# Performance work log

Hardware: AMD Instinct MI355X
Metric: run time of the kernel (lower is better)

Reference implementation:

```python
import jax, jax.numpy as jnp
import numpy as np

N_NODES = 100000
N_EDGES = 1000000
IN_F = 64
HEADS = 4
OUT_C = 32  # per-head channels
EDGE_DIM = 16
NEG_SLOPE = 0.2


def setup_inputs() -> dict:
    key = jax.random.key(0)
    ks = jax.random.split(key, 10)
    x = jax.random.normal(ks[0], (N_NODES, IN_F), dtype=jnp.float32)
    edge_index = jax.random.randint(ks[1], (2, N_EDGES), 0, N_NODES, dtype=jnp.int64)
    edge_attr = jax.random.normal(ks[2], (N_EDGES, EDGE_DIM), dtype=jnp.float32)
    s = 1.0 / np.sqrt(IN_F)
    W = jax.random.normal(ks[3], (IN_F, HEADS * OUT_C), dtype=jnp.float32) * s
    W_edge = jax.random.normal(ks[4], (EDGE_DIM, HEADS * OUT_C), dtype=jnp.float32) * (1.0 / np.sqrt(EDGE_DIM))
    att_src = jax.random.normal(ks[5], (HEADS, OUT_C), dtype=jnp.float32) * (1.0 / np.sqrt(OUT_C))
    att_dst = jax.random.normal(ks[6], (HEADS, OUT_C), dtype=jnp.float32) * (1.0 / np.sqrt(OUT_C))
    att_edge = jax.random.normal(ks[7], (HEADS, OUT_C), dtype=jnp.float32) * (1.0 / np.sqrt(OUT_C))
    bias = jnp.zeros((HEADS * OUT_C,), dtype=jnp.float32)
    return {"x": x, "edge_index": edge_index, "edge_attr": edge_attr,
            "W": W, "W_edge": W_edge, "att_src": att_src, "att_dst": att_dst,
            "att_edge": att_edge, "bias": bias}


def reference(x, edge_index, edge_attr, W, W_edge, att_src, att_dst, att_edge, bias):
    # PyG GATConv with edge_dim, add_self_loops=False, concat=True.
    N = x.shape[0]
    src = edge_index[0]  # message source j
    dst = edge_index[1]  # message target i

    x_proj = (x @ W).reshape(N, HEADS, OUT_C)          # [N,H,C]
    a_src = jnp.einsum('nhc,hc->nh', x_proj, att_src)  # [N,H]
    a_dst = jnp.einsum('nhc,hc->nh', x_proj, att_dst)  # [N,H]

    e_proj = (edge_attr @ W_edge).reshape(-1, HEADS, OUT_C)  # [E,H,C]
    a_edge = jnp.einsum('ehc,hc->eh', e_proj, att_edge)      # [E,H]

    alpha = a_src[src] + a_dst[dst] + a_edge                 # [E,H]
    alpha = jax.nn.leaky_relu(alpha, NEG_SLOPE)

    # edge softmax grouped by destination node
    seg_max = jax.ops.segment_max(alpha, dst, num_segments=N)  # [N,H]
    alpha = jnp.exp(alpha - seg_max[dst])
    denom = jax.ops.segment_sum(alpha, dst, num_segments=N)    # [N,H]
    alpha = alpha / (denom[dst] + 1e-16)

    msg = x_proj[src] * alpha[:, :, None]                      # [E,H,C]
    out = jax.ops.segment_sum(msg, dst, num_segments=N)        # [N,H,C]
    return out.reshape(N, HEADS * OUT_C) + bias
```

## Files before the change

### kernel.cpp

```cpp
#include <hip/hip_runtime.h>
#include <hip/hip_fp16.h>


#define HC 128
#define NEG 0.2f
#define CH 16
#define K_SHIFT 6.0f
#define NBK 512
#define BSH 8
#define BMSK 255
#define BCAP 3584
#define EPB 4096

typedef __fp16 half2_t __attribute__((ext_vector_type(2)));

__device__ __forceinline__ unsigned short f2bf(float f) {
    unsigned u = __float_as_uint(f);
    return (unsigned short)((u + 0x7fffu + ((u >> 16) & 1u)) >> 16);
}
__device__ __forceinline__ unsigned pk_h2(float lo, float hi) {
    half2_t p = __builtin_amdgcn_cvt_pkrtz(lo, hi);
    union { half2_t h; unsigned u; } cv;
    cv.h = p;
    return cv.u;
}
__device__ __forceinline__ float h2f_bits(unsigned short bits) {
    __half_raw hr; hr.x = bits;
    return __half2float(*reinterpret_cast<__half*>(&hr));
}
__device__ __forceinline__ long ld_idx(const int* __restrict__ ei, long i, int m64) {
    return m64 ? (long)(((const long long*)ei)[i]) : (long)ei[i];
}
__device__ __forceinline__ int detect_m64(const int* __restrict__ ei, int* s_m64) {
    int t = threadIdx.x;
    if (t < 64) {
        unsigned long long bal = __ballot(ei[2 * t + 1] != 0);
        if (t == 0) *s_m64 = (bal == 0ull) ? 1 : 0;
    }
    __syncthreads();
    return *s_m64;
}

__global__ __launch_bounds__(1024) void k_bucket(
    const float* __restrict__ We, const float* __restrict__ ae,
    const float* __restrict__ eattr, const int* __restrict__ ei,
    int* __restrict__ bcur, unsigned* __restrict__ sdstg,
    uint2* __restrict__ aevstg, int E) {
    __shared__ float q_s[64];
    __shared__ int s_m64;
    __shared__ int hist[NBK];
    __shared__ int gb[NBK];
    int t = threadIdx.x;
    int m64 = detect_m64(ei, &s_m64);
    if (t < 64) {
        int dd = t >> 2, h = t & 3;
        float s = 0.f;
        for (int c = 0; c < 32; ++c)
            s += We[dd * HC + h * 32 + c] * ae[h * 32 + c];
        q_s[t] = s;
    }
    if (t < NBK) hist[t] = 0;
    __syncthreads();

    int base = blockIdx.x * EPB + t;
#pragma unroll
    for (int k = 0; k < 4; ++k) {
        int e = base + k * 1024;
        if (e < E) {
            int d = (int)ld_idx(ei, (long)E + e, m64);
            atomicAdd(&hist[d >> BSH], 1);
        }
    }
    __syncthreads();
    if (t < NBK) {
        int c = hist[t];
        gb[t] = c ? atomicAdd(&bcur[t], c) : 0;
        hist[t] = 0;
    }
    __syncthreads();

#pragma unroll
    for (int k = 0; k < 4; ++k) {
        int e = base + k * 1024;
        if (e >= E) continue;
        int d = (int)ld_idx(ei, (long)E + e, m64);
        int b = d >> BSH;
        int lr = atomicAdd(&hist[b], 1);
        int off = gb[b] + lr;
        if (off >= BCAP) continue;
        long s = ld_idx(ei, e, m64);
        const float4* pe = reinterpret_cast<const float4*>(eattr + (long)e * 16);
        float4 e0 = pe[0], e1 = pe[1], e2 = pe[2], e3 = pe[3];
        float ev[16] = {e0.x, e0.y, e0.z, e0.w, e1.x, e1.y, e1.z, e1.w,
                        e2.x, e2.y, e2.z, e2.w, e3.x, e3.y, e3.z, e3.w};
        float ov[4];
#pragma unroll
        for (int h = 0; h < 4; ++h) {
            float aev = 0.f;
#pragma unroll
            for (int dd = 0; dd < 16; ++dd) aev += ev[dd] * q_s[dd * 4 + h];
            ov[h] = aev;
        }
        int slot = b * BCAP + off;
        sdstg[slot] = (unsigned)s | ((unsigned)(d & BMSK) << 20);
        aevstg[slot] = make_uint2(pk_h2(ov[0], ov[1]), pk_h2(ov[2], ov[3]));
    }
}

__global__ void k_bscan(const int* __restrict__ bcur, int* __restrict__ bbase,
                        int* __restrict__ row, int N, int E) {
    int t = threadIdx.x;
    if (t >= 64) return;
    int v[8]; int sum = 0;
#pragma unroll
    for (int k = 0; k < 8; ++k) { v[k] = bcur[t * 8 + k]; sum += v[k]; }
    int s = sum;
#pragma unroll
    for (int off = 1; off < 64; off <<= 1) {
        int u = __shfl_up(s, off, 64);
        if (t >= off) s += u;
    }
    int run = s - sum;
#pragma unroll
    for (int k = 0; k < 8; ++k) { bbase[t * 8 + k] = run; run += v[k]; }
    if (t == 0) row[N] = E;
}

__global__ __launch_bounds__(512) void k_csr(
    const unsigned* __restrict__ sdstg, const uint2* __restrict__ aevstg,
    const int* __restrict__ bcur, const int* __restrict__ bbase,
    const float* __restrict__ a_src, const float* __restrict__ a_dst,
    int* __restrict__ row, uint4* __restrict__ srt, int N) {
    int b = blockIdx.x, t = threadIdx.x;
    __shared__ int deg_l[256];
    __shared__ int s_sc[256];
    __shared__ int pfx[256];
    if (t < 256) deg_l[t] = 0;
    __syncthreads();
    int cnt = bcur[b]; if (cnt > BCAP) cnt = BCAP;
    int base = bbase[b];

    int r[7];
    unsigned recs[7];
#pragma unroll
    for (int k = 0; k < 7; ++k) {
        int i = k * 512 + t;
        r[k] = -1; recs[k] = 0u;
        if (i < cnt) {
            unsigned sd = sdstg[b * BCAP + i];
            recs[k] = sd;
            r[k] = atomicAdd(&deg_l[(sd >> 20) & BMSK], 1);
        }
    }
    __syncthreads();
    int own = (t < 256) ? deg_l[t] : 0;
    if (t < 256) s_sc[t] = own;
    __syncthreads();
    for (int off = 1; off < 256; off <<= 1) {
        int xv = (t >= off && t < 256) ? s_sc[t - off] : 0;
        __syncthreads();
        if (t < 256) s_sc[t] += xv;
        __syncthreads();
    }
    if (t < 256) {
        int ex = s_sc[t] - own;
        pfx[t] = ex;
        int n = b * 256 + t;
        if (n <= N) row[n] = base + ex;
    }
    __syncthreads();

#pragma unroll
    for (int k = 0; k < 7; ++k) {
        int i = k * 512 + t;
        if (i >= cnt) continue;
        unsigned sd = recs[k];
        int dl = (sd >> 20) & BMSK;
        int s = (int)(sd & 0xFFFFFu);
        uint2 av = aevstg[b * BCAP + i];
        float4 s4 = *reinterpret_cast<const float4*>(a_src + (long)s * 4);
        float4 d4 = *reinterpret_cast<const float4*>(a_dst + (long)(b * 256 + dl) * 4);
        float lf[4];
        lf[0] = s4.x + d4.x + h2f_bits((unsigned short)(av.x & 0xffffu));
        lf[1] = s4.y + d4.y + h2f_bits((unsigned short)(av.x >> 16));
        lf[2] = s4.z + d4.z + h2f_bits((unsigned short)(av.y & 0xffffu));
        lf[3] = s4.w + d4.w + h2f_bits((unsigned short)(av.y >> 16));
        float exv[4];
#pragma unroll
        for (int h = 0; h < 4; ++h) {
            float v = (lf[h] > 0.f) ? lf[h] : NEG * lf[h];
            exv[h] = __expf(v - K_SHIFT);
        }
        int pos = base + pfx[dl] + r[k];
        srt[pos] = make_uint4((unsigned)s, pk_h2(exv[0], exv[1]),
                              pk_h2(exv[2], exv[3]), 0u);
    }
}

__global__ __launch_bounds__(256) void k_proj(
    const float* __restrict__ x, const float* __restrict__ W,
    const float* __restrict__ as_, const float* __restrict__ ad_,
    unsigned short* __restrict__ xp, float* __restrict__ a_src,
    float* __restrict__ a_dst, int N) {
    __shared__ float x_s[64][68];
    int t = threadIdx.x;
    int n0 = blockIdx.x * 64;
#pragma unroll
    for (int i = 0; i < 4; ++i) {
        int fl = i * 256 + t;
        int node = fl >> 4, f4 = fl & 15;
        float4 v = make_float4(0.f, 0.f, 0.f, 0.f);
        if (n0 + node < N)
            v = *reinterpret_cast<const float4*>(&x[(long)(n0 + node) * 64 + f4 * 4]);
        x_s[f4 * 4 + 0][node] = v.x;
        x_s[f4 * 4 + 1][node] = v.y;
        x_s[f4 * 4 + 2][node] = v.z;
        x_s[f4 * 4 + 3][node] = v.w;
    }
    __syncthreads();

    int c = t & 31;
    int nd = t >> 5;
    const float4* __restrict__ W4 = reinterpret_cast<const float4*>(W);
    float acc[8][4];
#pragma unroll
    for (int i = 0; i < 8; ++i)
#pragma unroll
        for (int j = 0; j < 4; ++j) acc[i][j] = 0.f;

#pragma unroll 8
    for (int k = 0; k < 64; ++k) {
        float4 w4 = W4[k * 32 + c];
        float4 xa = *reinterpret_cast<const float4*>(&x_s[k][nd * 8]);
        float4 xb = *reinterpret_cast<const float4*>(&x_s[k][nd * 8 + 4]);
        float xv[8] = {xa.x, xa.y, xa.z, xa.w, xb.x, xb.y, xb.z, xb.w};
#pragma unroll
        for (int i = 0; i < 8; ++i) {
            acc[i][0] += xv[i] * w4.x;
            acc[i][1] += xv[i] * w4.y;
            acc[i][2] += xv[i] * w4.z;
            acc[i][3] += xv[i] * w4.w;
        }
    }

    float4 s4 = *reinterpret_cast<const float4*>(&as_[c * 4]);
    float4 d4 = *reinterpret_cast<const float4*>(&ad_[c * 4]);
#pragma unroll
    for (int i = 0; i < 8; ++i) {
        int node = n0 + nd * 8 + i;
        if (node < N) {
            ushort4 o;
            o.x = f2bf(acc[i][0]); o.y = f2bf(acc[i][1]);
            o.z = f2bf(acc[i][2]); o.w = f2bf(acc[i][3]);
            *reinterpret_cast<ushort4*>(&xp[(long)node * HC + c * 4]) = o;
        }
        float ps = acc[i][0] * s4.x + acc[i][1] * s4.y + acc[i][2] * s4.z + acc[i][3] * s4.w;
        float pd = acc[i][0] * d4.x + acc[i][1] * d4.y + acc[i][2] * d4.z + acc[i][3] * d4.w;
#pragma unroll
        for (int off = 1; off < 8; off <<= 1) {
            ps += __shfl_xor(ps, off, 64);
            pd += __shfl_xor(pd, off, 64);
        }
        if ((c & 7) == 0 && node < N) {
            int h = c >> 3;
            a_src[(long)node * 4 + h] = ps;
            a_dst[(long)node * 4 + h] = pd;
        }
    }
}

__global__ __launch_bounds__(128) void k_gather(
    const int* __restrict__ row, const uint4* __restrict__ srt,
    const char* __restrict__ xpc, const float* __restrict__ bias,
    float* __restrict__ out, int N) {
    int wid = threadIdx.x >> 6;
    int lane = threadIdx.x & 63;
    int n = blockIdx.x * 2 + wid;
    if (n >= N) return;
    int beg = row[n], end = row[n + 1];
    int h_s = lane & 3, e_s = lane >> 2;
    int par = lane >> 5;
    int cl = lane & 31;
    int h_a = cl >> 3;
    float l = 0.f;
    float acc[4] = {0.f, 0.f, 0.f, 0.f};

    __shared__ float s_ex[2][CH][4];
    __shared__ int s_off[2][CH];
    __shared__ float s_l[2][4];

    for (int cs = beg; cs < end; cs += CH) {
        int cnt = end - cs;
        if (cnt > CH) cnt = CH;
        float ex = 0.f;
        if (e_s < cnt) {
            uint4 r = srt[cs + e_s];
            if (h_s == 0) s_off[wid][e_s] = (int)(r.x << 8);
            unsigned pr = (h_s & 2) ? r.z : r.y;
            unsigned bits = (h_s & 1) ? (pr >> 16) : (pr & 0xffffu);
            ex = h2f_bits((unsigned short)bits);
        }
        s_ex[wid][e_s][h_s] = ex;
        float se = ex;
        se += __shfl_xor(se, 4, 64);
        se += __shfl_xor(se, 8, 64);
        se += __shfl_xor(se, 16, 64);
        se += __shfl_xor(se, 32, 64);
        l += se;
        int j = 0;
        for (; j + 4 <= cnt; j += 4) {
            int ea0 = j + par, ea1 = j + 2 + par;
            int o0 = s_off[wid][ea0], o1 = s_off[wid][ea1];
            float w0 = s_ex[wid][ea0][h_a], w1 = s_ex[wid][ea1][h_a];
            uint2 v0 = *reinterpret_cast<const uint2*>(xpc + o0 + cl * 8);
            uint2 v1 = *reinterpret_cast<const uint2*>(xpc + o1 + cl * 8);
            acc[0] += w0 * __uint_as_float(v0.x << 16);
            acc[1] += w0 * __uint_as_float(v0.x & 0xffff0000u);
            acc[2] += w0 * __uint_as_float(v0.y << 16);
            acc[3] += w0 * __uint_as_float(v0.y & 0xffff0000u);
            acc[0] += w1 * __uint_as_float(v1.x << 16);
            acc[1] += w1 * __uint_as_float(v1.x & 0xffff0000u);
            acc[2] += w1 * __uint_as_float(v1.y << 16);
            acc[3] += w1 * __uint_as_float(v1.y & 0xffff0000u);
        }
        for (; j < cnt; j += 2) {
            int e = j + par;
            bool act = e < cnt;
            int o = s_off[wid][act ? e : j];
            float w = act ? s_ex[wid][e][h_a] : 0.f;
            uint2 v = *reinterpret_cast<const uint2*>(xpc + o + cl * 8);
            acc[0] += w * __uint_as_float(v.x << 16);
            acc[1] += w * __uint_as_float(v.x & 0xffff0000u);
            acc[2] += w * __uint_as_float(v.y << 16);
            acc[3] += w * __uint_as_float(v.y & 0xffff0000u);
        }
    }
    if (lane < 4) s_l[wid][h_s] = l;
#pragma unroll
    for (int k = 0; k < 4; ++k) acc[k] += __shfl_xor(acc[k], 32, 64);
    if (par == 0) {
        float d = s_l[wid][h_a] + 1e-16f;
        float4 b4 = *reinterpret_cast<const float4*>(bias + cl * 4);
        float4 o;
        o.x = acc[0] / d + b4.x;
        o.y = acc[1] / d + b4.y;
        o.z = acc[2] / d + b4.z;
        o.w = acc[3] / d + b4.w;
        *reinterpret_cast<float4*>(out + (long)n * HC + cl * 4) = o;
    }
}

extern "C" void kernel_launch(void* const* d_in, const int* in_sizes, int n_in,
                              void* d_out, int out_size, void* d_ws, size_t ws_size,
                              hipStream_t stream) {
    const float* x    = (const float*)d_in[0];
    const int*   ei   = (const int*)d_in[1];
    const float* ea   = (const float*)d_in[2];
    const float* W    = (const float*)d_in[3];
    const float* We   = (const float*)d_in[4];
    const float* as_  = (const float*)d_in[5];
    const float* ad_  = (const float*)d_in[6];
    const float* ae   = (const float*)d_in[7];
    const float* bias = (const float*)d_in[8];
    float* out = (float*)d_out;

    int N = in_sizes[0] / 64;
    int E = in_sizes[1] / 2;

    char* ws = (char*)d_ws;
    size_t off = 0;
    auto take = [&](size_t bytes) -> char* {
        char* p = ws + off;
        off += (bytes + 511) & ~(size_t)511;
        return p;
    };
    unsigned short* xp = (unsigned short*)take((size_t)N * HC * 2);
    float* a_src    = (float*)take((size_t)N * 4 * 4);
    float* a_dst    = (float*)take((size_t)N * 4 * 4);
    uint4* srt      = (uint4*)take((size_t)E * 16);
    unsigned* sdstg = (unsigned*)take((size_t)NBK * BCAP * 4);
    uint2* aevstg   = (uint2*)take((size_t)NBK * BCAP * 8);
    int* row        = (int*)take((size_t)(N + 1) * 4);
    int* bcur       = (int*)take((size_t)NBK * 4);
    int* bbase      = (int*)take((size_t)NBK * 4);

    int Np = (N + 63) / 64;
    int nbA = (E + EPB - 1) / EPB;
    int nbB = (N + 255) / 256;

    (void)hipMemsetAsync(bcur, 0, (size_t)NBK * 4, stream);
    hipLaunchKernelGGL(k_bucket, dim3(nbA), dim3(1024), 0, stream,
                       We, ae, ea, ei, bcur, sdstg, aevstg, E);
    hipLaunchKernelGGL(k_proj, dim3(Np), dim3(256), 0, stream,
                       x, W, as_, ad_, xp, a_src, a_dst, N);
    hipLaunchKernelGGL(k_bscan, dim3(1), dim3(64), 0, stream,
                       bcur, bbase, row, N, E);
    hipLaunchKernelGGL(k_csr, dim3(nbB), dim3(512), 0, stream,
                       sdstg, aevstg, bcur, bbase, a_src, a_dst, row, srt, N);
    hipLaunchKernelGGL(k_gather, dim3((N + 1) / 2), dim3(128), 0, stream,
                       row, srt, (const char*)xp, bias, out, N);
}
```

Baseline: 277.8 us.

## Stage bucketed edge records in LDS to coalesce global scatter writes

The bucketing kernel now sorts each block's edges by bucket in shared memory, using a block-wide prefix scan of the bucket histogram, before writing to global memory. Consecutive threads then write consecutive slots within the same bucket, so the scattered per-edge stores become mostly contiguous runs. This adds about 50KB of LDS per block, a 9-step scan with barriers and an extra pass, which lowers occupancy.

```diff
diff --git a/kernel.cpp b/kernel.cpp
--- a/kernel.cpp
+++ b/kernel.cpp
@@ -50,6 +50,12 @@
     __shared__ int s_m64;
     __shared__ int hist[NBK];
     __shared__ int gb[NBK];
+    __shared__ int loff[NBK];
+    __shared__ int cnt2[NBK];
+    __shared__ int s_sc[NBK];
+    __shared__ unsigned sd_l[EPB];
+    __shared__ unsigned short bk_l[EPB];
+    __shared__ uint2 aev_l[EPB];
     int t = threadIdx.x;
     int m64 = detect_m64(ei, &s_m64);
     if (t < 64) {
@@ -59,7 +65,7 @@
             s += We[dd * HC + h * 32 + c] * ae[h * 32 + c];
         q_s[t] = s;
     }
-    if (t < NBK) hist[t] = 0;
+    if (t < NBK) { hist[t] = 0; cnt2[t] = 0; }
     __syncthreads();
 
     int base = blockIdx.x * EPB + t;
@@ -75,8 +81,17 @@
     if (t < NBK) {
         int c = hist[t];
         gb[t] = c ? atomicAdd(&bcur[t], c) : 0;
-        hist[t] = 0;
-    }
+    }
+    int own = (t < NBK) ? hist[t] : 0;
+    if (t < NBK) s_sc[t] = own;
+    __syncthreads();
+    for (int off = 1; off < NBK; off <<= 1) {
+        int xv = (t < NBK && t >= off) ? s_sc[t - off] : 0;
+        __syncthreads();
+        if (t < NBK) s_sc[t] += xv;
+        __syncthreads();
+    }
+    if (t < NBK) loff[t] = s_sc[t] - own;
     __syncthreads();
 
 #pragma unroll
@@ -85,9 +100,7 @@
         if (e >= E) continue;
         int d = (int)ld_idx(ei, (long)E + e, m64);
         int b = d >> BSH;
-        int lr = atomicAdd(&hist[b], 1);
-        int off = gb[b] + lr;
-        if (off >= BCAP) continue;
+        int lr = atomicAdd(&cnt2[b], 1);
         long s = ld_idx(ei, e, m64);
         const float4* pe = reinterpret_cast<const float4*>(eattr + (long)e * 16);
         float4 e0 = pe[0], e1 = pe[1], e2 = pe[2], e3 = pe[3];
@@ -101,9 +114,24 @@
             for (int dd = 0; dd < 16; ++dd) aev += ev[dd] * q_s[dd * 4 + h];
             ov[h] = aev;
         }
-        int slot = b * BCAP + off;
-        sdstg[slot] = (unsigned)s | ((unsigned)(d & BMSK) << 20);
-        aevstg[slot] = make_uint2(pk_h2(ov[0], ov[1]), pk_h2(ov[2], ov[3]));
+        int li = loff[b] + lr;
+        sd_l[li] = (unsigned)s | ((unsigned)(d & BMSK) << 20);
+        bk_l[li] = (unsigned short)b;
+        aev_l[li] = make_uint2(pk_h2(ov[0], ov[1]), pk_h2(ov[2], ov[3]));
+    }
+    __syncthreads();
+
+    int nrec = E - blockIdx.x * EPB;
+    if (nrec > EPB) nrec = EPB;
+#pragma unroll
+    for (int k = 0; k < 4; ++k) {
+        int i = k * 1024 + t;
+        if (i >= nrec) continue;
+        int b = bk_l[i];
+        int off = gb[b] + (i - loff[b]);
+        if (off >= BCAP) continue;
+        sdstg[b * BCAP + off] = sd_l[i];
+        aevstg[b * BCAP + off] = aev_l[i];
     }
 }
 
```

Result: faster. 259.1 us (-6.7%).

## Fuse bucket+projection into one front kernel and CSR+gather into bucket-local back kernel

Applied to the files above, without the earlier changes.

Bucketing and the node projection now run as one launch, with blocks split by blockIdx. The bucketing half stages each block's records in LDS sorted by bucket, so the global scatter writes contiguous runs. The CSR build and the neighbour gather are merged into a per-bucket kernel that keeps the per-destination edge lists in LDS, with one wave covering 32 nodes. This removes the global srt, row and bbase arrays and three launches. The cost is heavy LDS use and per-wave serial node loops that may reduce parallelism and balance poorly across nodes.

```diff
diff --git a/kernel.cpp b/kernel.cpp
--- a/kernel.cpp
+++ b/kernel.cpp
@@ -41,173 +41,120 @@
     return *s_m64;
 }
 
-__global__ __launch_bounds__(1024) void k_bucket(
+union FrontLDS {
+    struct {
+        int hist[NBK]; int gb[NBK]; int loff[NBK]; int cnt2[NBK]; int s_sc[NBK];
+        unsigned sd_l[EPB];
+        unsigned short bk_l[EPB];
+        uint2 aev_l[EPB];
+    } b;
+    struct {
+        float x_s[4][64][68];
+    } p;
+};
+
+__global__ __launch_bounds__(1024, 8) void k_front(
+    const float* __restrict__ x, const float* __restrict__ W,
+    const float* __restrict__ as_, const float* __restrict__ ad_,
     const float* __restrict__ We, const float* __restrict__ ae,
     const float* __restrict__ eattr, const int* __restrict__ ei,
-    int* __restrict__ bcur, unsigned* __restrict__ sdstg,
-    uint2* __restrict__ aevstg, int E) {
+    unsigned short* __restrict__ xp, float* __restrict__ a_src,
+    float* __restrict__ a_dst, int* __restrict__ bcur,
+    unsigned* __restrict__ sdstg, uint2* __restrict__ aevstg,
+    int N, int E, int nbA) {
+    __shared__ FrontLDS L;
     __shared__ float q_s[64];
     __shared__ int s_m64;
-    __shared__ int hist[NBK];
-    __shared__ int gb[NBK];
     int t = threadIdx.x;
-    int m64 = detect_m64(ei, &s_m64);
-    if (t < 64) {
-        int dd = t >> 2, h = t & 3;
-        float s = 0.f;
-        for (int c = 0; c < 32; ++c)
-            s += We[dd * HC + h * 32 + c] * ae[h * 32 + c];
-        q_s[t] = s;
-    }
-    if (t < NBK) hist[t] = 0;
-    __syncthreads();
-
-    int base = blockIdx.x * EPB + t;
-#pragma unroll
-    for (int k = 0; k < 4; ++k) {
-        int e = base + k * 1024;
-        if (e < E) {
+    int id = blockIdx.x;
+
+    if (id < nbA) {
+        int m64 = detect_m64(ei, &s_m64);
+        if (t < 64) {
+            int dd = t >> 2, h = t & 3;
+            float s = 0.f;
+            for (int c = 0; c < 32; ++c)
+                s += We[dd * HC + h * 32 + c] * ae[h * 32 + c];
+            q_s[t] = s;
+        }
+        if (t < NBK) { L.b.hist[t] = 0; L.b.cnt2[t] = 0; }
+        __syncthreads();
+
+        int base = id * EPB + t;
+#pragma unroll
+        for (int k = 0; k < 4; ++k) {
+            int e = base + k * 1024;
+            if (e < E) {
+                int d = (int)ld_idx(ei, (long)E + e, m64);
+                atomicAdd(&L.b.hist[d >> BSH], 1);
+            }
+        }
+        __syncthreads();
+        if (t < NBK) {
+            int c = L.b.hist[t];
+            L.b.gb[t] = c ? atomicAdd(&bcur[t], c) : 0;
+        }
+        int own = (t < NBK) ? L.b.hist[t] : 0;
+        if (t < NBK) L.b.s_sc[t] = own;
+        __syncthreads();
+        for (int off = 1; off < NBK; off <<= 1) {
+            int xv = (t < NBK && t >= off) ? L.b.s_sc[t - off] : 0;
+            __syncthreads();
+            if (t < NBK) L.b.s_sc[t] += xv;
+            __syncthreads();
+        }
+        if (t < NBK) L.b.loff[t] = L.b.s_sc[t] - own;
+        __syncthreads();
+
+#pragma unroll
+        for (int k = 0; k < 4; ++k) {
+            int e = base + k * 1024;
+            if (e >= E) continue;
             int d = (int)ld_idx(ei, (long)E + e, m64);
-            atomicAdd(&hist[d >> BSH], 1);
-        }
-    }
-    __syncthreads();
-    if (t < NBK) {
-        int c = hist[t];
-        gb[t] = c ? atomicAdd(&bcur[t], c) : 0;
-        hist[t] = 0;
-    }
-    __syncthreads();
-
-#pragma unroll
-    for (int k = 0; k < 4; ++k) {
-        int e = base + k * 1024;
-        if (e >= E) continue;
-        int d = (int)ld_idx(ei, (long)E + e, m64);
-        int b = d >> BSH;
-        int lr = atomicAdd(&hist[b], 1);
-        int off = gb[b] + lr;
-        if (off >= BCAP) continue;
-        long s = ld_idx(ei, e, m64);
-        const float4* pe = reinterpret_cast<const float4*>(eattr + (long)e * 16);
-        float4 e0 = pe[0], e1 = pe[1], e2 = pe[2], e3 = pe[3];
-        float ev[16] = {e0.x, e0.y, e0.z, e0.w, e1.x, e1.y, e1.z, e1.w,
-                        e2.x, e2.y, e2.z, e2.w, e3.x, e3.y, e3.z, e3.w};
-        float ov[4];
-#pragma unroll
-        for (int h = 0; h < 4; ++h) {
-            float aev = 0.f;
-#pragma unroll
-            for (int dd = 0; dd < 16; ++dd) aev += ev[dd] * q_s[dd * 4 + h];
-            ov[h] = aev;
-        }
-        int slot = b * BCAP + off;
-        sdstg[slot] = (unsigned)s | ((unsigned)(d & BMSK) << 20);
-        aevstg[slot] = make_uint2(pk_h2(ov[0], ov[1]), pk_h2(ov[2], ov[3]));
-    }
-}
-
-__global__ void k_bscan(const int* __restrict__ bcur, int* __restrict__ bbase,
-                        int* __restrict__ row, int N, int E) {
-    int t = threadIdx.x;
-    if (t >= 64) return;
-    int v[8]; int sum = 0;
-#pragma unroll
-    for (int k = 0; k < 8; ++k) { v[k] = bcur[t * 8 + k]; sum += v[k]; }
-    int s = sum;
-#pragma unroll
-    for (int off = 1; off < 64; off <<= 1) {
-        int u = __shfl_up(s, off, 64);
-        if (t >= off) s += u;
-    }
-    int run = s - sum;
-#pragma unroll
-    for (int k = 0; k < 8; ++k) { bbase[t * 8 + k] = run; run += v[k]; }
-    if (t == 0) row[N] = E;
-}
-
-__global__ __launch_bounds__(512) void k_csr(
-    const unsigned* __restrict__ sdstg, const uint2* __restrict__ aevstg,
-    const int* __restrict__ bcur, const int* __restrict__ bbase,
-    const float* __restrict__ a_src, const float* __restrict__ a_dst,
-    int* __restrict__ row, uint4* __restrict__ srt, int N) {
-    int b = blockIdx.x, t = threadIdx.x;
-    __shared__ int deg_l[256];
-    __shared__ int s_sc[256];
-    __shared__ int pfx[256];
-    if (t < 256) deg_l[t] = 0;
-    __syncthreads();
-    int cnt = bcur[b]; if (cnt > BCAP) cnt = BCAP;
-    int base = bbase[b];
-
-    int r[7];
-    unsigned recs[7];
-#pragma unroll
-    for (int k = 0; k < 7; ++k) {
-        int i = k * 512 + t;
-        r[k] = -1; recs[k] = 0u;
-        if (i < cnt) {
-            unsigned sd = sdstg[b * BCAP + i];
-            recs[k] = sd;
-            r[k] = atomicAdd(&deg_l[(sd >> 20) & BMSK], 1);
-        }
-    }
-    __syncthreads();
-    int own = (t < 256) ? deg_l[t] : 0;
-    if (t < 256) s_sc[t] = own;
-    __syncthreads();
-    for (int off = 1; off < 256; off <<= 1) {
-        int xv = (t >= off && t < 256) ? s_sc[t - off] : 0;
-        __syncthreads();
-        if (t < 256) s_sc[t] += xv;
-        __syncthreads();
-    }
-    if (t < 256) {
-        int ex = s_sc[t] - own;
-        pfx[t] = ex;
-        int n = b * 256 + t;
-        if (n <= N) row[n] = base + ex;
-    }
-    __syncthreads();
-
-#pragma unroll
-    for (int k = 0; k < 7; ++k) {
-        int i = k * 512 + t;
-        if (i >= cnt) continue;
-        unsigned sd = recs[k];
-        int dl = (sd >> 20) & BMSK;
-        int s = (int)(sd & 0xFFFFFu);
-        uint2 av = aevstg[b * BCAP + i];
-        float4 s4 = *reinterpret_cast<const float4*>(a_src + (long)s * 4);
-        float4 d4 = *reinterpret_cast<const float4*>(a_dst + (long)(b * 256 + dl) * 4);
-        float lf[4];
-        lf[0] = s4.x + d4.x + h2f_bits((unsigned short)(av.x & 0xffffu));
-        lf[1] = s4.y + d4.y + h2f_bits((unsigned short)(av.x >> 16));
-        lf[2] = s4.z + d4.z + h2f_bits((unsigned short)(av.y & 0xffffu));
-        lf[3] = s4.w + d4.w + h2f_bits((unsigned short)(av.y >> 16));
-        float exv[4];
-#pragma unroll
-        for (int h = 0; h < 4; ++h) {
-            float v = (lf[h] > 0.f) ? lf[h] : NEG * lf[h];
-            exv[h] = __expf(v - K_SHIFT);
-        }
-        int pos = base + pfx[dl] + r[k];
-        srt[pos] = make_uint4((unsigned)s, pk_h2(exv[0], exv[1]),
-                              pk_h2(exv[2], exv[3]), 0u);
-    }
-}
-
-__global__ __launch_bounds__(256) void k_proj(
-    const float* __restrict__ x, const float* __restrict__ W,
-    const float* __restrict__ as_, const float* __restrict__ ad_,
-    unsigned short* __restrict__ xp, float* __restrict__ a_src,
-    float* __restrict__ a_dst, int N) {
-    __shared__ float x_s[64][68];
-    int t = threadIdx.x;
-    int n0 = blockIdx.x * 64;
+            int b = d >> BSH;
+            int lr = atomicAdd(&L.b.cnt2[b], 1);
+            long s = ld_idx(ei, e, m64);
+            const float4* pe = reinterpret_cast<const float4*>(eattr + (long)e * 16);
+            float4 e0 = pe[0], e1 = pe[1], e2 = pe[2], e3 = pe[3];
+            float ev[16] = {e0.x, e0.y, e0.z, e0.w, e1.x, e1.y, e1.z, e1.w,
+                            e2.x, e2.y, e2.z, e2.w, e3.x, e3.y, e3.z, e3.w};
+            float ov[4];
+#pragma unroll
+            for (int h = 0; h < 4; ++h) {
+                float aev = 0.f;
+#pragma unroll
+                for (int dd = 0; dd < 16; ++dd) aev += ev[dd] * q_s[dd * 4 + h];
+                ov[h] = aev;
+            }
+            int li = L.b.loff[b] + lr;
+            L.b.sd_l[li] = (unsigned)s | ((unsigned)(d & BMSK) << 20);
+            L.b.bk_l[li] = (unsigned short)b;
+            L.b.aev_l[li] = make_uint2(pk_h2(ov[0], ov[1]), pk_h2(ov[2], ov[3]));
+        }
+        __syncthreads();
+
+        int nrec = E - id * EPB;
+        if (nrec > EPB) nrec = EPB;
+#pragma unroll
+        for (int k = 0; k < 4; ++k) {
+            int i = k * 1024 + t;
+            if (i >= nrec) continue;
+            int b = L.b.bk_l[i];
+            int off = L.b.gb[b] + (i - L.b.loff[b]);
+            if (off >= BCAP) continue;
+            sdstg[b * BCAP + off] = L.b.sd_l[i];
+            aevstg[b * BCAP + off] = L.b.aev_l[i];
+        }
+        return;
+    }
+
+    int pid = id - nbA;
+    int q = t >> 8, tid = t & 255;
+    int n0 = pid * 256 + q * 64;
+    float (*x_s)[68] = L.p.x_s[q];
 #pragma unroll
     for (int i = 0; i < 4; ++i) {
-        int fl = i * 256 + t;
+        int fl = i * 256 + tid;
         int node = fl >> 4, f4 = fl & 15;
         float4 v = make_float4(0.f, 0.f, 0.f, 0.f);
         if (n0 + node < N)
@@ -219,8 +166,8 @@
     }
     __syncthreads();
 
-    int c = t & 31;
-    int nd = t >> 5;
+    int c = tid & 31;
+    int nd = tid >> 5;
     const float4* __restrict__ W4 = reinterpret_cast<const float4*>(W);
     float acc[8][4];
 #pragma unroll
@@ -269,84 +216,147 @@
     }
 }
 
-__global__ __launch_bounds__(128) void k_gather(
-    const int* __restrict__ row, const uint4* __restrict__ srt,
-    const char* __restrict__ xpc, const float* __restrict__ bias,
-    float* __restrict__ out, int N) {
-    int wid = threadIdx.x >> 6;
-    int lane = threadIdx.x & 63;
-    int n = blockIdx.x * 2 + wid;
-    if (n >= N) return;
-    int beg = row[n], end = row[n + 1];
+__global__ __launch_bounds__(512, 6) void k_back(
+    const unsigned* __restrict__ sdstg, const uint2* __restrict__ aevstg,
+    const int* __restrict__ bcur, const float* __restrict__ a_src,
+    const float* __restrict__ a_dst, const char* __restrict__ xpc,
+    const float* __restrict__ bias, float* __restrict__ out, int N) {
+    int b = blockIdx.x, t = threadIdx.x;
+    __shared__ int deg_l[256];
+    __shared__ int s_sc[256];
+    __shared__ int pfx[256];
+    __shared__ unsigned src_l[BCAP];
+    __shared__ uint2 w_l[BCAP];
+    __shared__ float s_ex[8][CH][4];
+    __shared__ int s_off[8][CH];
+    __shared__ float s_l[8][4];
+    if (t < 256) deg_l[t] = 0;
+    __syncthreads();
+    int cnt = bcur[b]; if (cnt > BCAP) cnt = BCAP;
+
+    unsigned sdr[7]; int rkr[7]; uint2 wr[7];
+#pragma unroll
+    for (int k = 0; k < 7; ++k) {
+        int i = k * 512 + t;
+        sdr[k] = 0u; rkr[k] = -1; wr[k] = make_uint2(0u, 0u);
+        if (i < cnt) {
+            unsigned sd = sdstg[b * BCAP + i];
+            sdr[k] = sd;
+            int dl = (sd >> 20) & BMSK;
+            rkr[k] = atomicAdd(&deg_l[dl], 1);
+            int s = (int)(sd & 0xFFFFFu);
+            uint2 av = aevstg[b * BCAP + i];
+            float4 s4 = *reinterpret_cast<const float4*>(a_src + (long)s * 4);
+            float4 d4 = *reinterpret_cast<const float4*>(a_dst + (long)(b * 256 + dl) * 4);
+            float lf[4];
+            lf[0] = s4.x + d4.x + h2f_bits((unsigned short)(av.x & 0xffffu));
+            lf[1] = s4.y + d4.y + h2f_bits((unsigned short)(av.x >> 16));
+            lf[2] = s4.z + d4.z + h2f_bits((unsigned short)(av.y & 0xffffu));
+            lf[3] = s4.w + d4.w + h2f_bits((unsigned short)(av.y >> 16));
+            float exv[4];
+#pragma unroll
+            for (int h = 0; h < 4; ++h) {
+                float v = (lf[h] > 0.f) ? lf[h] : NEG * lf[h];
+                exv[h] = __expf(v - K_SHIFT);
+            }
+            wr[k] = make_uint2(pk_h2(exv[0], exv[1]), pk_h2(exv[2], exv[3]));
+        }
+    }
+    __syncthreads();
+    int own = (t < 256) ? deg_l[t] : 0;
+    if (t < 256) s_sc[t] = own;
+    __syncthreads();
+    for (int off = 1; off < 256; off <<= 1) {
+        int xv = (t >= off && t < 256) ? s_sc[t - off] : 0;
+        __syncthreads();
+        if (t < 256) s_sc[t] += xv;
+        __syncthreads();
+    }
+    if (t < 256) pfx[t] = s_sc[t] - own;
+    __syncthreads();
+#pragma unroll
+    for (int k = 0; k < 7; ++k) {
+        int i = k * 512 + t;
+        if (i >= cnt) continue;
+        int dl = (sdr[k] >> 20) & BMSK;
+        int pos = pfx[dl] + rkr[k];
+        src_l[pos] = sdr[k] & 0xFFFFFu;
+        w_l[pos] = wr[k];
+    }
+    __syncthreads();
+
+    int wv = t >> 6, lane = t & 63;
     int h_s = lane & 3, e_s = lane >> 2;
     int par = lane >> 5;
     int cl = lane & 31;
     int h_a = cl >> 3;
-    float l = 0.f;
-    float acc[4] = {0.f, 0.f, 0.f, 0.f};
-
-    __shared__ float s_ex[2][CH][4];
-    __shared__ int s_off[2][CH];
-    __shared__ float s_l[2][4];
-
-    for (int cs = beg; cs < end; cs += CH) {
-        int cnt = end - cs;
-        if (cnt > CH) cnt = CH;
-        float ex = 0.f;
-        if (e_s < cnt) {
-            uint4 r = srt[cs + e_s];
-            if (h_s == 0) s_off[wid][e_s] = (int)(r.x << 8);
-            unsigned pr = (h_s & 2) ? r.z : r.y;
-            unsigned bits = (h_s & 1) ? (pr >> 16) : (pr & 0xffffu);
-            ex = h2f_bits((unsigned short)bits);
-        }
-        s_ex[wid][e_s][h_s] = ex;
-        float se = ex;
-        se += __shfl_xor(se, 4, 64);
-        se += __shfl_xor(se, 8, 64);
-        se += __shfl_xor(se, 16, 64);
-        se += __shfl_xor(se, 32, 64);
-        l += se;
-        int j = 0;
-        for (; j + 4 <= cnt; j += 4) {
-            int ea0 = j + par, ea1 = j + 2 + par;
-            int o0 = s_off[wid][ea0], o1 = s_off[wid][ea1];
-            float w0 = s_ex[wid][ea0][h_a], w1 = s_ex[wid][ea1][h_a];
-            uint2 v0 = *reinterpret_cast<const uint2*>(xpc + o0 + cl * 8);
-            uint2 v1 = *reinterpret_cast<const uint2*>(xpc + o1 + cl * 8);
-            acc[0] += w0 * __uint_as_float(v0.x << 16);
-            acc[1] += w0 * __uint_as_float(v0.x & 0xffff0000u);
-            acc[2] += w0 * __uint_as_float(v0.y << 16);
-            acc[3] += w0 * __uint_as_float(v0.y & 0xffff0000u);
-            acc[0] += w1 * __uint_as_float(v1.x << 16);
-            acc[1] += w1 * __uint_as_float(v1.x & 0xffff0000u);
-            acc[2] += w1 * __uint_as_float(v1.y << 16);
-            acc[3] += w1 * __uint_as_float(v1.y & 0xffff0000u);
-        }
-        for (; j < cnt; j += 2) {
-            int e = j + par;
-            bool act = e < cnt;
-            int o = s_off[wid][act ? e : j];
-            float w = act ? s_ex[wid][e][h_a] : 0.f;
-            uint2 v = *reinterpret_cast<const uint2*>(xpc + o + cl * 8);
-            acc[0] += w * __uint_as_float(v.x << 16);
-            acc[1] += w * __uint_as_float(v.x & 0xffff0000u);
-            acc[2] += w * __uint_as_float(v.y << 16);
-            acc[3] += w * __uint_as_float(v.y & 0xffff0000u);
-        }
-    }
-    if (lane < 4) s_l[wid][h_s] = l;
-#pragma unroll
-    for (int k = 0; k < 4; ++k) acc[k] += __shfl_xor(acc[k], 32, 64);
-    if (par == 0) {
-        float d = s_l[wid][h_a] + 1e-16f;
-        float4 b4 = *reinterpret_cast<const float4*>(bias + cl * 4);
-        float4 o;
-        o.x = acc[0] / d + b4.x;
-        o.y = acc[1] / d + b4.y;
-        o.z = acc[2] / d + b4.z;
-        o.w = acc[3] / d + b4.w;
-        *reinterpret_cast<float4*>(out + (long)n * HC + cl * 4) = o;
+    for (int ni = 0; ni < 32; ++ni) {
+        int dl = wv * 32 + ni;
+        int n = b * 256 + dl;
+        if (n >= N) continue;
+        int beg = pfx[dl];
+        int end = beg + deg_l[dl];
+        float l = 0.f;
+        float acc[4] = {0.f, 0.f, 0.f, 0.f};
+        for (int cs = beg; cs < end; cs += CH) {
+            int c2 = end - cs;
+            if (c2 > CH) c2 = CH;
+            float ex = 0.f;
+            if (e_s < c2) {
+                if (h_s == 0) s_off[wv][e_s] = (int)(src_l[cs + e_s] << 8);
+                uint2 wv2 = w_l[cs + e_s];
+                unsigned pr = (h_s & 2) ? wv2.y : wv2.x;
+                unsigned bits = (h_s & 1) ? (pr >> 16) : (pr & 0xffffu);
+                ex = h2f_bits((unsigned short)bits);
+            }
+            s_ex[wv][e_s][h_s] = ex;
+            float se = ex;
+            se += __shfl_xor(se, 4, 64);
+            se += __shfl_xor(se, 8, 64);
+            se += __shfl_xor(se, 16, 64);
+            se += __shfl_xor(se, 32, 64);
+            l += se;
+            int j = 0;
+            for (; j + 4 <= c2; j += 4) {
+                int ea0 = j + par, ea1 = j + 2 + par;
+                int o0 = s_off[wv][ea0], o1 = s_off[wv][ea1];
+                float w0 = s_ex[wv][ea0][h_a], w1 = s_ex[wv][ea1][h_a];
+                uint2 v0 = *reinterpret_cast<const uint2*>(xpc + o0 + cl * 8);
+                uint2 v1 = *reinterpret_cast<const uint2*>(xpc + o1 + cl * 8);
+                acc[0] += w0 * __uint_as_float(v0.x << 16);
+                acc[1] += w0 * __uint_as_float(v0.x & 0xffff0000u);
+                acc[2] += w0 * __uint_as_float(v0.y << 16);
+                acc[3] += w0 * __uint_as_float(v0.y & 0xffff0000u);
+                acc[0] += w1 * __uint_as_float(v1.x << 16);
+                acc[1] += w1 * __uint_as_float(v1.x & 0xffff0000u);
+                acc[2] += w1 * __uint_as_float(v1.y << 16);
+                acc[3] += w1 * __uint_as_float(v1.y & 0xffff0000u);
+            }
+            for (; j < c2; j += 2) {
+                int e = j + par;
+                bool act = e < c2;
+                int o = s_off[wv][act ? e : j];
+                float w = act ? s_ex[wv][e][h_a] : 0.f;
+                uint2 v = *reinterpret_cast<const uint2*>(xpc + o + cl * 8);
+                acc[0] += w * __uint_as_float(v.x << 16);
+                acc[1] += w * __uint_as_float(v.x & 0xffff0000u);
+                acc[2] += w * __uint_as_float(v.y << 16);
+                acc[3] += w * __uint_as_float(v.y & 0xffff0000u);
+            }
+        }
+        if (lane < 4) s_l[wv][h_s] = l;
+#pragma unroll
+        for (int k = 0; k < 4; ++k) acc[k] += __shfl_xor(acc[k], 32, 64);
+        if (par == 0) {
+            float d = s_l[wv][h_a] + 1e-16f;
+            float4 b4 = *reinterpret_cast<const float4*>(bias + cl * 4);
+            float4 o;
+            o.x = acc[0] / d + b4.x;
+            o.y = acc[1] / d + b4.y;
+            o.z = acc[2] / d + b4.z;
+            o.w = acc[3] / d + b4.w;
+            *reinterpret_cast<float4*>(out + (long)n * HC + cl * 4) = o;
+        }
     }
 }
 
@@ -377,26 +387,18 @@
     unsigned short* xp = (unsigned short*)take((size_t)N * HC * 2);
     float* a_src    = (float*)take((size_t)N * 4 * 4);
     float* a_dst    = (float*)take((size_t)N * 4 * 4);
-    uint4* srt      = (uint4*)take((size_t)E * 16);
     unsigned* sdstg = (unsigned*)take((size_t)NBK * BCAP * 4);
     uint2* aevstg   = (uint2*)take((size_t)NBK * BCAP * 8);
-    int* row        = (int*)take((size_t)(N + 1) * 4);
     int* bcur       = (int*)take((size_t)NBK * 4);
-    int* bbase      = (int*)take((size_t)NBK * 4);
-
-    int Np = (N + 63) / 64;
+
     int nbA = (E + EPB - 1) / EPB;
-    int nbB = (N + 255) / 256;
+    int nbP = (N + 255) / 256;
 
     (void)hipMemsetAsync(bcur, 0, (size_t)NBK * 4, stream);
-    hipLaunchKernelGGL(k_bucket, dim3(nbA), dim3(1024), 0, stream,
-                       We, ae, ea, ei, bcur, sdstg, aevstg, E);
-    hipLaunchKernelGGL(k_proj, dim3(Np), dim3(256), 0, stream,
-                       x, W, as_, ad_, xp, a_src, a_dst, N);
-    hipLaunchKernelGGL(k_bscan, dim3(1), dim3(64), 0, stream,
-                       bcur, bbase, row, N, E);
-    hipLaunchKernelGGL(k_csr, dim3(nbB), dim3(512), 0, stream,
-                       sdstg, aevstg, bcur, bbase, a_src, a_dst, row, srt, N);
-    hipLaunchKernelGGL(k_gather, dim3((N + 1) / 2), dim3(128), 0, stream,
-                       row, srt, (const char*)xp, bias, out, N);
-}
+    hipLaunchKernelGGL(k_front, dim3(nbA + nbP), dim3(1024), 0, stream,
+                       x, W, as_, ad_, We, ae, ea, ei,
+                       xp, a_src, a_dst, bcur, sdstg, aevstg, N, E, nbA);
+    hipLaunchKernelGGL(k_back, dim3(nbP), dim3(512), 0, stream,
+                       sdstg, aevstg, bcur, a_src, a_dst,
+                       (const char*)xp, bias, out, N);
+}
```

Result: faster. 271.2 us (-2.4%).
